# Kernel optimization log

Measured on AMD Instinct MI355X. Metric: run time of the kernel, lower is better.

## Reference

```python
import jax, jax.numpy as jnp
import numpy as np

R = 1.1
SCALE = 100.0
BUMP_STEPS = 32
NUM_THETAS = 32
NUM_FEATURES = 128
N_NODES = 200000
NUM_GRAPHS = 128


def setup_inputs() -> dict:
    key = jax.random.key(0)
    k1, k2, k3 = jax.random.split(key, 3)
    x = jax.random.normal(k1, (N_NODES, NUM_FEATURES), dtype=jnp.float32)
    batch = jnp.sort(jax.random.randint(k2, (N_NODES,), 0, NUM_GRAPHS, dtype=jnp.int64))
    v = jax.random.uniform(k3, (NUM_THETAS, NUM_FEATURES), dtype=jnp.float32) - 0.5
    return {"x": x, "batch": batch, "num_graphs": NUM_GRAPHS, "v": v}


def reference(x, batch, num_graphs, v):
    # nh: node heights along each direction theta -> [N, T]
    nh = x @ v.T
    # linspace over filtration values -> [S]
    lin = jnp.linspace(-R, R, BUMP_STEPS, dtype=nh.dtype)
    # bump: sigmoid difference; second point is the constant pad value R
    # ecc: [N, S, T]  (node-major so segment_sum reduces the leading axis)
    ecc = (jax.nn.sigmoid(SCALE * (lin[None, :, None] - nh[:, None, :]))
           - jax.nn.sigmoid(SCALE * (lin - R))[None, :, None])
    # scatter-add per graph label -> [ng, S, T] == index_add over dim1 then movedim(0,1)
    ect = jax.ops.segment_sum(ecc, batch, num_segments=num_graphs)
    return ect
```

## Files before the change

kernel.cpp:

```cpp
#include <hip/hip_runtime.h>
#include <hip/hip_bf16.h>
#include <math.h>

#define N_NODES 200000
#define NF 128
#define NT 32
#define NS 32
#define NG 128
#define ATILE 64
#define NTILES 30

typedef short bf16x8 __attribute__((ext_vector_type(8)));
typedef float floatx4 __attribute__((ext_vector_type(4)));

__device__ __forceinline__ float rcp_fast(float x) { return __builtin_amdgcn_rcpf(x); }

__device__ __forceinline__ unsigned short bf16_bits(float f) {
    __hip_bfloat16 h = __float2bfloat16(f);
    unsigned short u; __builtin_memcpy(&u, &h, 2); return u;
}
__device__ __forceinline__ float bf16_val(unsigned short u) {
    unsigned v = (unsigned)u << 16; float f; __builtin_memcpy(&f, &v, 4); return f;
}
__device__ __forceinline__ void split1(float f, unsigned short& h, unsigned short& l) {
    h = bf16_bits(f);
    l = bf16_bits(f - bf16_val(h));
}
__device__ __forceinline__ void split8(float4 a, float4 b, bf16x8& h8, bf16x8& l8) {
    unsigned short h[8], l[8];
    split1(a.x, h[0], l[0]); split1(a.y, h[1], l[1]);
    split1(a.z, h[2], l[2]); split1(a.w, h[3], l[3]);
    split1(b.x, h[4], l[4]); split1(b.y, h[5], l[5]);
    split1(b.z, h[6], l[6]); split1(b.w, h[7], l[7]);
    h8 = (bf16x8){(short)h[0],(short)h[1],(short)h[2],(short)h[3],
                  (short)h[4],(short)h[5],(short)h[6],(short)h[7]};
    l8 = (bf16x8){(short)l[0],(short)l[1],(short)l[2],(short)l[3],
                  (short)l[4],(short)l[5],(short)l[6],(short)l[7]};
}

__device__ __forceinline__ void deposit(float* corr, int t, float z, float Lw, float C1) {
    float s0f = ceilf(z - 1.0f);
    int   s0  = (int)s0f;
    float e0  = __builtin_amdgcn_exp2f(Lw * (z - s0f));
    float e1  = e0 * C1;
    float f0  = rcp_fast(1.0f + e0);
    float f1  = rcp_fast(1.0f + e1);
    int tb = t * 32;
    atomicAdd(&corr[tb + (max(s0, 0) ^ t)], f0);
    int sB = s0 + 1; if (sB < 32) atomicAdd(&corr[tb + (sB ^ t)], f1 - f0);
    int sC = s0 + 2; if (sC < 32) atomicAdd(&corr[tb + (sC ^ t)], 1.0f - f1);
}

__global__ __launch_bounds__(256)
void starts_vprep(const int* __restrict__ batch, int* __restrict__ starts,
                  const float* __restrict__ v,
                  unsigned short* __restrict__ vth, unsigned short* __restrict__ vtl,
                  int do_vprep)
{
    if (blockIdx.x == gridDim.x - 1) {
        if (!do_vprep) return;
        const int tid = threadIdx.x;
        #pragma unroll
        for (int j = 0; j < 4; ++j) {
            int idx4 = tid * 4 + j;
            float4 val = ((const float4*)v)[idx4];
            unsigned short h0,h1,h2,h3,l0,l1,l2,l3;
            split1(val.x, h0, l0); split1(val.y, h1, l1);
            split1(val.z, h2, l2); split1(val.w, h3, l3);
            uint2 hh, ll;
            hh.x = (unsigned)h0 | ((unsigned)h1 << 16); hh.y = (unsigned)h2 | ((unsigned)h3 << 16);
            ll.x = (unsigned)l0 | ((unsigned)l1 << 16); ll.y = (unsigned)l2 | ((unsigned)l3 << 16);
            *(uint2*)&vth[idx4 * 4] = hh;
            *(uint2*)&vtl[idx4 * 4] = ll;
        }
        return;
    }
    int i = blockIdx.x * 256 + threadIdx.x;
    if (i >= N_NODES) return;
    int b    = batch[i];
    int prev = (i == 0) ? -1 : batch[i - 1];
    for (int g = prev + 1; g <= b; ++g) starts[g] = i;
    if (i == N_NODES - 1)
        for (int g = b + 1; g <= NG; ++g) starts[g] = N_NODES;
}

__global__ __launch_bounds__(256, 8)
void ect_tile(const float* __restrict__ x,
              const float* __restrict__ v,
              const int* __restrict__ starts,
              const unsigned short* __restrict__ vth,
              const unsigned short* __restrict__ vtl,
              float* __restrict__ partials,
              float* __restrict__ out,
              int use_ws)
{
    __shared__ __align__(16) unsigned short vh[NT * 128];
    __shared__ __align__(16) unsigned short vl[NT * 128];
    __shared__ float corr[NT * 32];

    const int tid  = threadIdx.x;
    const int t    = blockIdx.x;
    const int g    = blockIdx.y;
    const int w    = tid >> 6;
    const int lane = tid & 63;
    const int mrow = lane & 15;
    const int quad = lane >> 4;

    const int start = starts[g];
    const int count = starts[g + 1] - start;
    const int slot  = g * NTILES + t;

    if (t * ATILE >= count) {
        if (use_ws) {
            float4 z4 = {0.f, 0.f, 0.f, 0.f};
            *(float4*)&partials[(size_t)slot * 1024 + tid * 4] = z4;
        }
        return;
    }
    const int base   = start + t * ATILE;
    const int nvalid = min(ATILE, count - t * ATILE);

    const int gi = min(base + w * 16 + mrow, N_NODES - 1);
    const float* __restrict__ xrow = x + (size_t)gi * NF + quad * 8;
    float4 xa0 = *(const float4*)&xrow[0];
    float4 xa1 = *(const float4*)&xrow[4];
    float4 xa2 = *(const float4*)&xrow[32];
    float4 xa3 = *(const float4*)&xrow[36];

    if (use_ws) {
        #pragma unroll
        for (int j = 0; j < 2; ++j) {
            int u    = j * 256 + tid;
            int row  = u >> 4;
            int s16p = (u & 15) ^ (row & 15);
            *(uint4*)&vh[row * 128 + s16p * 8] = *(const uint4*)&vth[u * 8];
            *(uint4*)&vl[row * 128 + s16p * 8] = *(const uint4*)&vtl[u * 8];
        }
    } else {
        #pragma unroll
        for (int j = 0; j < 4; ++j) {
            int idx4 = j * 256 + tid;
            int row  = idx4 >> 5;
            int col8 = idx4 & 31;
            int col8p = (((col8 >> 1) ^ (row & 15)) << 1) | (col8 & 1);
            float4 val = *(const float4*)&v[(size_t)row * NF + col8 * 4];
            unsigned short h0,h1,h2,h3,l0,l1,l2,l3;
            split1(val.x, h0, l0); split1(val.y, h1, l1);
            split1(val.z, h2, l2); split1(val.w, h3, l3);
            uint2 hh, ll;
            hh.x = (unsigned)h0 | ((unsigned)h1 << 16); hh.y = (unsigned)h2 | ((unsigned)h3 << 16);
            ll.x = (unsigned)l0 | ((unsigned)l1 << 16); ll.y = (unsigned)l2 | ((unsigned)l3 << 16);
            *(uint2*)&vh[row * 128 + col8p * 4] = hh;
            *(uint2*)&vl[row * 128 + col8p * 4] = ll;
        }
    }
    #pragma unroll
    for (int i = tid; i < NT * 32; i += 256) corr[i] = 0.0f;

    bf16x8 ah0, al0, ah1, al1;
    split8(xa0, xa1, ah0, al0);
    split8(xa2, xa3, ah1, al1);
    float4 xb0 = *(const float4*)&xrow[64];
    float4 xb1 = *(const float4*)&xrow[68];
    float4 xb2 = *(const float4*)&xrow[96];
    float4 xb3 = *(const float4*)&xrow[100];
    __syncthreads();

    floatx4 acc0 = {0.f, 0.f, 0.f, 0.f};
    floatx4 acc1 = {0.f, 0.f, 0.f, 0.f};
    const int o0 = mrow * 128;
    const int o1 = o0 + 2048;
    #pragma unroll
    for (int slice = 0; slice < 4; ++slice) {
        if (slice == 2) {
            split8(xb0, xb1, ah0, al0);
            split8(xb2, xb3, ah1, al1);
        }
        bf16x8 a_h = (slice & 1) ? ah1 : ah0;
        bf16x8 a_l = (slice & 1) ? al1 : al0;
        int sp = (((quad | (slice << 2)) ^ mrow) << 3);
        bf16x8 bh0 = *(bf16x8*)&vh[o0 + sp];
        bf16x8 bl0 = *(bf16x8*)&vl[o0 + sp];
        bf16x8 bh1 = *(bf16x8*)&vh[o1 + sp];
        bf16x8 bl1 = *(bf16x8*)&vl[o1 + sp];
        acc0 = __builtin_amdgcn_mfma_f32_16x16x32_bf16(a_h, bh0, acc0, 0, 0, 0);
        acc0 = __builtin_amdgcn_mfma_f32_16x16x32_bf16(a_h, bl0, acc0, 0, 0, 0);
        acc0 = __builtin_amdgcn_mfma_f32_16x16x32_bf16(a_l, bh0, acc0, 0, 0, 0);
        acc1 = __builtin_amdgcn_mfma_f32_16x16x32_bf16(a_h, bh1, acc1, 0, 0, 0);
        acc1 = __builtin_amdgcn_mfma_f32_16x16x32_bf16(a_h, bl1, acc1, 0, 0, 0);
        acc1 = __builtin_amdgcn_mfma_f32_16x16x32_bf16(a_l, bh1, acc1, 0, 0, 0);
    }

    const float inv_dlin = 14.090909090909092f;
    const float Lw       = 10.23848093f;
    const float dlin     = 2.2f / 31.0f;
    const float L        = 144.26950408889634f;
    const float C1       = 8.2777115e-04f;

    float c0 = 0.f, c1 = 0.f;
    const int nloc = w * 16 + quad * 4;
    #pragma unroll
    for (int reg = 0; reg < 4; ++reg) {
        if (nloc + reg < nvalid) {
            {
                float z = fmaf(acc0[reg], inv_dlin, 15.5f);
                if (z <= -1.0f)      c0 += 1.0f;
                else if (z < 32.0f)  deposit(corr, mrow, z, Lw, C1);
            }
            {
                float z = fmaf(acc1[reg], inv_dlin, 15.5f);
                if (z <= -1.0f)      c1 += 1.0f;
                else if (z < 32.0f)  deposit(corr, 16 + mrow, z, Lw, C1);
            }
        }
    }
    if (c0 != 0.f) atomicAdd(&corr[mrow * 32 + (0 ^ mrow)], c0);
    if (c1 != 0.f) atomicAdd(&corr[(16 + mrow) * 32 + (0 ^ (16 + mrow))], c1);
    __syncthreads();

    {
        const int grp = tid >> 5;
        const int sc  = tid & 31;
        for (int row = grp; row < NT; row += 8) {
            float val = corr[row * 32 + (sc ^ row)];
            #pragma unroll
            for (int d = 1; d < 32; d <<= 1) {
                float nbr = __shfl_up(val, d, 32);
                if (sc >= d) val += nbr;
            }
            corr[row * 32 + (sc ^ row)] = val;
        }
    }
    __syncthreads();

    const float cnt  = (float)nvalid;
    const int   s    = tid >> 3;
    const int   ft0  = (tid & 7) * 4;
    const float lin_s = -1.1f + (float)s * dlin;
    const float cs    = rcp_fast(1.0f + __builtin_amdgcn_exp2f(L * (1.1f - lin_s)));
    float4 r;
    r.x = corr[(ft0 + 0) * 32 + (s ^ (ft0 + 0))] - cnt * cs;
    r.y = corr[(ft0 + 1) * 32 + (s ^ (ft0 + 1))] - cnt * cs;
    r.z = corr[(ft0 + 2) * 32 + (s ^ (ft0 + 2))] - cnt * cs;
    r.w = corr[(ft0 + 3) * 32 + (s ^ (ft0 + 3))] - cnt * cs;
    if (use_ws) {
        *(float4*)&partials[(size_t)slot * 1024 + tid * 4] = r;
    } else {
        float* o = out + (size_t)g * (NS * NT) + tid * 4;
        atomicAdd(&o[0], r.x); atomicAdd(&o[1], r.y);
        atomicAdd(&o[2], r.z); atomicAdd(&o[3], r.w);
    }
}

__global__ __launch_bounds__(256)
void reduce_partials(const float* __restrict__ partials, float* __restrict__ out) {
    const int g   = blockIdx.x;
    const int tid = threadIdx.x;
    const float4* p4 = (const float4*)partials;
    float4 acc = {0.f, 0.f, 0.f, 0.f};
    #pragma unroll
    for (int t = 0; t < NTILES; ++t) {
        float4 v = p4[(size_t)(g * NTILES + t) * 256 + tid];
        acc.x += v.x; acc.y += v.y; acc.z += v.z; acc.w += v.w;
    }
    ((float4*)out)[(size_t)g * 256 + tid] = acc;
}

extern "C" void kernel_launch(void* const* d_in, const int* in_sizes, int n_in,
                              void* d_out, int out_size, void* d_ws, size_t ws_size,
                              hipStream_t stream) {
    const float* x     = (const float*)d_in[0];
    const int*   batch = (const int*)d_in[1];
    const float* v     = (const float*)d_in[3];
    float*       out   = (float*)d_out;

    int*            starts   = (int*)d_ws;
    unsigned short* vth      = (unsigned short*)((char*)d_ws + 1024);
    unsigned short* vtl      = (unsigned short*)((char*)d_ws + 1024 + 8192);
    float*          partials = (float*)((char*)d_ws + 1024 + 16384);
    const size_t need = 1024 + 16384 + (size_t)NG * NTILES * 1024 * sizeof(float);
    const int use_ws  = (ws_size >= need) ? 1 : 0;

    const int nsb = (N_NODES + 255) / 256 + 1;
    starts_vprep<<<dim3(nsb), dim3(256), 0, stream>>>(batch, starts, v, vth, vtl, use_ws);
    if (use_ws) {
        ect_tile<<<dim3(NTILES, NG), dim3(256), 0, stream>>>(x, v, starts, vth, vtl,
                                                             partials, out, 1);
        reduce_partials<<<dim3(NG), dim3(256), 0, stream>>>(partials, out);
    } else {
        hipMemsetAsync(d_out, 0, (size_t)out_size * sizeof(float), stream);
        ect_tile<<<dim3(NTILES, NG), dim3(256), 0, stream>>>(x, v, starts, vth, vtl,
                                                             partials, out, 0);
    }
}
```

Before: 175.0 us.

## Process 128 nodes per block with prefetched second sub-tile

Doubles the per-block node tile from 64 to 128 and halves the tile count per graph, so each block runs two GEMM-plus-deposit passes over the same shared v tile and correction buffer. Loads for the second sub-tile are issued early, before the first sub-tile's deposit phase, so global latency overlaps compute. This amortizes v staging, corr zeroing, the prefix scan and the partial write-out over twice as many nodes. In exchange it uses more registers (launch bounds lowered to 7) and yields fewer blocks, which may reduce parallelism on small graphs.

```diff
diff --git a/kernel.cpp b/kernel.cpp
--- a/kernel.cpp
+++ b/kernel.cpp
@@ -7,8 +7,8 @@
 #define NT 32
 #define NS 32
 #define NG 128
-#define ATILE 64
-#define NTILES 30
+#define ATILE 128
+#define NTILES 15
 
 typedef short bf16x8 __attribute__((ext_vector_type(8)));
 typedef float floatx4 __attribute__((ext_vector_type(4)));
@@ -84,7 +84,7 @@
         for (int g = b + 1; g <= NG; ++g) starts[g] = N_NODES;
 }
 
-__global__ __launch_bounds__(256, 8)
+__global__ __launch_bounds__(256, 7)
 void ect_tile(const float* __restrict__ x,
               const float* __restrict__ v,
               const int* __restrict__ starts,
@@ -119,13 +119,17 @@
     }
     const int base   = start + t * ATILE;
     const int nvalid = min(ATILE, count - t * ATILE);
-
-    const int gi = min(base + w * 16 + mrow, N_NODES - 1);
-    const float* __restrict__ xrow = x + (size_t)gi * NF + quad * 8;
-    float4 xa0 = *(const float4*)&xrow[0];
-    float4 xa1 = *(const float4*)&xrow[4];
-    float4 xa2 = *(const float4*)&xrow[32];
-    float4 xa3 = *(const float4*)&xrow[36];
+    const bool doB   = (nvalid > 64);
+
+    const int rA  = w * 16 + mrow;
+    const int giA = min(base + rA,      N_NODES - 1);
+    const int giB = min(base + 64 + rA, N_NODES - 1);
+    const float* __restrict__ xrowA = x + (size_t)giA * NF + quad * 8;
+    const float* __restrict__ xrowB = x + (size_t)giB * NF + quad * 8;
+    float4 xa0 = *(const float4*)&xrowA[0];
+    float4 xa1 = *(const float4*)&xrowA[4];
+    float4 xa2 = *(const float4*)&xrowA[32];
+    float4 xa3 = *(const float4*)&xrowA[36];
 
     if (use_ws) {
         #pragma unroll
@@ -160,36 +164,11 @@
     bf16x8 ah0, al0, ah1, al1;
     split8(xa0, xa1, ah0, al0);
     split8(xa2, xa3, ah1, al1);
-    float4 xb0 = *(const float4*)&xrow[64];
-    float4 xb1 = *(const float4*)&xrow[68];
-    float4 xb2 = *(const float4*)&xrow[96];
-    float4 xb3 = *(const float4*)&xrow[100];
+    float4 xc0 = *(const float4*)&xrowA[64];
+    float4 xc1 = *(const float4*)&xrowA[68];
+    float4 xc2 = *(const float4*)&xrowA[96];
+    float4 xc3 = *(const float4*)&xrowA[100];
     __syncthreads();
-
-    floatx4 acc0 = {0.f, 0.f, 0.f, 0.f};
-    floatx4 acc1 = {0.f, 0.f, 0.f, 0.f};
-    const int o0 = mrow * 128;
-    const int o1 = o0 + 2048;
-    #pragma unroll
-    for (int slice = 0; slice < 4; ++slice) {
-        if (slice == 2) {
-            split8(xb0, xb1, ah0, al0);
-            split8(xb2, xb3, ah1, al1);
-        }
-        bf16x8 a_h = (slice & 1) ? ah1 : ah0;
-        bf16x8 a_l = (slice & 1) ? al1 : al0;
-        int sp = (((quad | (slice << 2)) ^ mrow) << 3);
-        bf16x8 bh0 = *(bf16x8*)&vh[o0 + sp];
-        bf16x8 bl0 = *(bf16x8*)&vl[o0 + sp];
-        bf16x8 bh1 = *(bf16x8*)&vh[o1 + sp];
-        bf16x8 bl1 = *(bf16x8*)&vl[o1 + sp];
-        acc0 = __builtin_amdgcn_mfma_f32_16x16x32_bf16(a_h, bh0, acc0, 0, 0, 0);
-        acc0 = __builtin_amdgcn_mfma_f32_16x16x32_bf16(a_h, bl0, acc0, 0, 0, 0);
-        acc0 = __builtin_amdgcn_mfma_f32_16x16x32_bf16(a_l, bh0, acc0, 0, 0, 0);
-        acc1 = __builtin_amdgcn_mfma_f32_16x16x32_bf16(a_h, bh1, acc1, 0, 0, 0);
-        acc1 = __builtin_amdgcn_mfma_f32_16x16x32_bf16(a_h, bl1, acc1, 0, 0, 0);
-        acc1 = __builtin_amdgcn_mfma_f32_16x16x32_bf16(a_l, bh1, acc1, 0, 0, 0);
-    }
 
     const float inv_dlin = 14.090909090909092f;
     const float Lw       = 10.23848093f;
@@ -197,20 +176,85 @@
     const float L        = 144.26950408889634f;
     const float C1       = 8.2777115e-04f;
 
+    const int o0 = mrow * 128;
+    const int o1 = o0 + 2048;
+    #define BSP(slice) ((((quad | ((slice) << 2)) ^ mrow) << 3))
+    #define GEMM_SLICES(aH, aL, sl0, sl1, A0, A1)                                     \
+        {                                                                             \
+            bf16x8 bh0 = *(bf16x8*)&vh[o0 + BSP(sl0)];                                \
+            bf16x8 bl0 = *(bf16x8*)&vl[o0 + BSP(sl0)];                                \
+            bf16x8 bh1 = *(bf16x8*)&vh[o1 + BSP(sl0)];                                \
+            bf16x8 bl1 = *(bf16x8*)&vl[o1 + BSP(sl0)];                                \
+            A0 = __builtin_amdgcn_mfma_f32_16x16x32_bf16(aH##0, bh0, A0, 0, 0, 0);    \
+            A0 = __builtin_amdgcn_mfma_f32_16x16x32_bf16(aH##0, bl0, A0, 0, 0, 0);    \
+            A0 = __builtin_amdgcn_mfma_f32_16x16x32_bf16(aL##0, bh0, A0, 0, 0, 0);    \
+            A1 = __builtin_amdgcn_mfma_f32_16x16x32_bf16(aH##0, bh1, A1, 0, 0, 0);    \
+            A1 = __builtin_amdgcn_mfma_f32_16x16x32_bf16(aH##0, bl1, A1, 0, 0, 0);    \
+            A1 = __builtin_amdgcn_mfma_f32_16x16x32_bf16(aL##0, bh1, A1, 0, 0, 0);    \
+            bh0 = *(bf16x8*)&vh[o0 + BSP(sl1)];                                       \
+            bl0 = *(bf16x8*)&vl[o0 + BSP(sl1)];                                       \
+            bh1 = *(bf16x8*)&vh[o1 + BSP(sl1)];                                       \
+            bl1 = *(bf16x8*)&vl[o1 + BSP(sl1)];                                       \
+            A0 = __builtin_amdgcn_mfma_f32_16x16x32_bf16(aH##1, bh0, A0, 0, 0, 0);    \
+            A0 = __builtin_amdgcn_mfma_f32_16x16x32_bf16(aH##1, bl0, A0, 0, 0, 0);    \
+            A0 = __builtin_amdgcn_mfma_f32_16x16x32_bf16(aL##1, bh0, A0, 0, 0, 0);    \
+            A1 = __builtin_amdgcn_mfma_f32_16x16x32_bf16(aH##1, bh1, A1, 0, 0, 0);    \
+            A1 = __builtin_amdgcn_mfma_f32_16x16x32_bf16(aH##1, bl1, A1, 0, 0, 0);    \
+            A1 = __builtin_amdgcn_mfma_f32_16x16x32_bf16(aL##1, bh1, A1, 0, 0, 0);    \
+        }
+
+    floatx4 acc0 = {0.f, 0.f, 0.f, 0.f};
+    floatx4 acc1 = {0.f, 0.f, 0.f, 0.f};
+    GEMM_SLICES(ah, al, 0, 1, acc0, acc1)
+
+    split8(xc0, xc1, ah0, al0);
+    split8(xc2, xc3, ah1, al1);
+    float4 xb0, xb1, xb2, xb3;
+    if (doB) {
+        xb0 = *(const float4*)&xrowB[0];
+        xb1 = *(const float4*)&xrowB[4];
+        xb2 = *(const float4*)&xrowB[32];
+        xb3 = *(const float4*)&xrowB[36];
+    }
+    GEMM_SLICES(ah, al, 2, 3, acc0, acc1)
+
     float c0 = 0.f, c1 = 0.f;
     const int nloc = w * 16 + quad * 4;
     #pragma unroll
     for (int reg = 0; reg < 4; ++reg) {
         if (nloc + reg < nvalid) {
-            {
-                float z = fmaf(acc0[reg], inv_dlin, 15.5f);
+            {   float z = fmaf(acc0[reg], inv_dlin, 15.5f);
                 if (z <= -1.0f)      c0 += 1.0f;
-                else if (z < 32.0f)  deposit(corr, mrow, z, Lw, C1);
-            }
-            {
-                float z = fmaf(acc1[reg], inv_dlin, 15.5f);
+                else if (z < 32.0f)  deposit(corr, mrow, z, Lw, C1); }
+            {   float z = fmaf(acc1[reg], inv_dlin, 15.5f);
                 if (z <= -1.0f)      c1 += 1.0f;
-                else if (z < 32.0f)  deposit(corr, 16 + mrow, z, Lw, C1);
+                else if (z < 32.0f)  deposit(corr, 16 + mrow, z, Lw, C1); }
+        }
+    }
+
+    if (doB) {
+        split8(xb0, xb1, ah0, al0);
+        split8(xb2, xb3, ah1, al1);
+        float4 xd0 = *(const float4*)&xrowB[64];
+        float4 xd1 = *(const float4*)&xrowB[68];
+        float4 xd2 = *(const float4*)&xrowB[96];
+        float4 xd3 = *(const float4*)&xrowB[100];
+        floatx4 bcc0 = {0.f, 0.f, 0.f, 0.f};
+        floatx4 bcc1 = {0.f, 0.f, 0.f, 0.f};
+        GEMM_SLICES(ah, al, 0, 1, bcc0, bcc1)
+        split8(xd0, xd1, ah0, al0);
+        split8(xd2, xd3, ah1, al1);
+        GEMM_SLICES(ah, al, 2, 3, bcc0, bcc1)
+        const int nlocB = 64 + nloc;
+        #pragma unroll
+        for (int reg = 0; reg < 4; ++reg) {
+            if (nlocB + reg < nvalid) {
+                {   float z = fmaf(bcc0[reg], inv_dlin, 15.5f);
+                    if (z <= -1.0f)      c0 += 1.0f;
+                    else if (z < 32.0f)  deposit(corr, mrow, z, Lw, C1); }
+                {   float z = fmaf(bcc1[reg], inv_dlin, 15.5f);
+                    if (z <= -1.0f)      c1 += 1.0f;
+                    else if (z < 32.0f)  deposit(corr, 16 + mrow, z, Lw, C1); }
             }
         }
     }
```

After: 195.2 us. 11.5% more time.
